# Optimization experiments

Hardware: AMD Instinct MI355X
Metric: run time of the kernel (lower is better)

The kernel has to match this reference:

```python
import jax, jax.numpy as jnp
from jax import lax
import numpy as np

NPOINT = 1024
RADIUS = 0.2
NSAMPLE = 32
MLP = [64, 64, 128]
EPS = 1e-5  # BatchNorm eps (torch default)


def setup_inputs() -> dict:
    key = jax.random.key(0)
    ks = jax.random.split(key, 2 + 3 * len(MLP))
    B, N = 8, 16384
    d = {
        "xyz": jax.random.uniform(ks[0], (B, N, 3), dtype=jnp.float32),
        "points": jax.random.normal(ks[1], (B, N, 3), dtype=jnp.float32),
    }
    cin = 6  # 3 (relative xyz) + 3 (point features)
    for i, cout in enumerate(MLP):
        d[f"w{i}"] = jax.random.normal(ks[2 + i], (cout, cin), dtype=jnp.float32) / np.float32(np.sqrt(cin))
        d[f"b{i}"] = jnp.zeros((cout,), jnp.float32)
        d[f"g{i}"] = jnp.ones((cout,), jnp.float32)
        d[f"be{i}"] = jnp.zeros((cout,), jnp.float32)
        cin = cout
    return d


def _fps(xyz, npoint):
    """Farthest point sampling. xyz: (B,N,3) -> idx (B,npoint) int32.
    Deterministic start at index 0 (original uses a random start)."""
    B, N, _ = xyz.shape

    def step(carry, _):
        distance, farthest = carry  # (B,N), (B,)
        centroid = jnp.take_along_axis(xyz, farthest[:, None, None], axis=1)  # (B,1,3)
        dist = jnp.sum((xyz - centroid) ** 2, axis=-1)  # (B,N)
        distance = jnp.minimum(distance, dist)
        nxt = jnp.argmax(distance, axis=-1).astype(jnp.int32)
        return (distance, nxt), farthest

    init = (jnp.full((B, N), 1e10, xyz.dtype), jnp.zeros((B,), jnp.int32))
    _, idxs = lax.scan(step, init, None, length=npoint)
    return idxs.T  # (B, npoint)


def _gather(points, idx):
    """points: (B,N,C), idx: (B,...) -> (B,...,C)."""
    return jax.vmap(lambda p, i: p[i])(points, idx)


def _ball_query(radius, nsample, xyz, new_xyz):
    B, N, _ = xyz.shape
    # (B,S,N) pairwise squared distances
    sqr = jnp.sum((new_xyz[:, :, None, :] - xyz[:, None, :, :]) ** 2, axis=-1)
    gidx = jnp.where(sqr > radius * radius, N, jnp.arange(N, dtype=jnp.int32))
    gidx = jnp.sort(gidx, axis=-1)[:, :, :nsample]  # (B,S,K)
    # replace out-of-ball (==N) with first in-ball index
    gidx = jnp.where(gidx == N, gidx[:, :, :1], gidx)
    return gidx


def reference(xyz, points, w0, b0, g0, be0, w1, b1, g1, be1, w2, b2, g2, be2):
    B, N, _ = xyz.shape
    fidx = _fps(xyz, NPOINT)                      # (B,S)
    new_xyz = _gather(xyz, fidx)                  # (B,S,3)
    gidx = _ball_query(RADIUS, NSAMPLE, xyz, new_xyz)  # (B,S,K)
    grouped_xyz = _gather(xyz, gidx) - new_xyz[:, :, None, :]  # (B,S,K,3)
    grouped_pts = _gather(points, gidx)           # (B,S,K,C)
    feat = jnp.concatenate([grouped_xyz, grouped_pts], axis=-1)  # (B,S,K,6)
    # shared MLP = 1x1 Conv2d + BatchNorm2d(train-mode stats) + ReLU
    for w, b, g, be in ((w0, b0, g0, be0), (w1, b1, g1, be1), (w2, b2, g2, be2)):
        feat = jnp.einsum('bskc,oc->bsko', feat, w) + b
        mu = feat.mean(axis=(0, 1, 2))
        var = feat.var(axis=(0, 1, 2))  # biased, as torch BN uses for normalization
        feat = jax.nn.relu(g * (feat - mu) * lax.rsqrt(var + EPS) + be)
    new_points = feat.max(axis=2)                 # max over nsample -> (B,S,C_out)
    return new_xyz, new_points
```

## Files before the change

kernel.cpp:

```cpp
#include <hip/hip_runtime.h>
#include <stdint.h>

#pragma clang fp contract(off)

#define NPT   16384
#define BB    8
#define SS    1024
#define KSAMP 32
#define PTOT  (BB*SS*KSAMP)
#define NGRP  (BB*SS)
#define R2    0.04f
#define EPSBN 1e-5f
#define INV_M 3.814697265625e-06f

#define OFF_S1 0
#define OFF_Q1 64
#define OFF_S2 128
#define OFF_Q2 192
#define OFF_S3 256
#define OFF_Q3 384
#define OFF_A1 512
#define OFF_C1 576
#define OFF_A2 640
#define OFF_C2 704
#define OFF_A3 768
#define OFF_C3 896
#define OFF_ZMAX 1024
#define OFF_FEAT (1024 + 1048576)

__device__ __forceinline__ float wave_sum(float v) {
#pragma unroll
  for (int off = 32; off; off >>= 1) v += __shfl_xor(v, off);
  return v;
}
__device__ __forceinline__ float half_max(float v) {
#pragma unroll
  for (int off = 16; off; off >>= 1) v = fmaxf(v, __shfl_xor(v, off));
  return v;
}

__device__ __forceinline__ float wave_max_dpp(float x) {
  int v = __float_as_int(x), t;
  t = __builtin_amdgcn_update_dpp(0, v, 0x111, 0xf, 0xf, true);
  v = __float_as_int(fmaxf(__int_as_float(v), __int_as_float(t)));
  t = __builtin_amdgcn_update_dpp(0, v, 0x112, 0xf, 0xf, true);
  v = __float_as_int(fmaxf(__int_as_float(v), __int_as_float(t)));
  t = __builtin_amdgcn_update_dpp(0, v, 0x114, 0xf, 0xf, true);
  v = __float_as_int(fmaxf(__int_as_float(v), __int_as_float(t)));
  t = __builtin_amdgcn_update_dpp(0, v, 0x118, 0xf, 0xf, true);
  v = __float_as_int(fmaxf(__int_as_float(v), __int_as_float(t)));
  t = __builtin_amdgcn_update_dpp(0, v, 0x142, 0xf, 0xf, true);
  v = __float_as_int(fmaxf(__int_as_float(v), __int_as_float(t)));
  t = __builtin_amdgcn_update_dpp(0, v, 0x143, 0xf, 0xf, true);
  v = __float_as_int(fmaxf(__int_as_float(v), __int_as_float(t)));
  return __int_as_float(__builtin_amdgcn_readlane(v, 63));
}

__global__ __launch_bounds__(1024)
void fps_kernel(const float* __restrict__ xyz, float* __restrict__ newxyz) {
  extern __shared__ float smem[];
  float2* sxy = (float2*)smem;
  __shared__ unsigned bmax[2];
  __shared__ unsigned long long wkey[2];
  const int b = blockIdx.x;
  const int t = threadIdx.x;
  const int lane = t & 63;
  const float* xb = xyz + (size_t)b * NPT * 3;

  float z[16], d[16];
#pragma unroll
  for (int j = 0; j < 16; ++j) {
    int p = j * 1024 + t;
    float xx = xb[3 * p];
    float yy = xb[3 * p + 1];
    float zz = xb[3 * p + 2];
    sxy[p] = make_float2(xx, yy);
    z[j] = zz;
    d[j] = 1e10f;
    asm volatile("" : "+v"(z[j]));
  }

  float cx = xb[0], cy = xb[1], cz = xb[2];
  if (t == 0) {
    bmax[0] = bmax[1] = 0u;
    wkey[0] = wkey[1] = ~0ull;
    float* o = newxyz + (size_t)b * SS * 3;
    o[0] = cx; o[1] = cy; o[2] = cz;
  }
  __syncthreads();

  const float2* pA = sxy + t;
  const float2* pB = sxy + t + 8192;

  for (int it = 1; it < SS; ++it) {
    const int buf = it & 1;
    float bv = 0.0f;
#pragma unroll
    for (int j = 0; j < 16; ++j) {
      float2 xy = (j < 8) ? pA[j * 1024] : pB[(j - 8) * 1024];
      float dx = xy.x - cx, dy = xy.y - cy, dz = z[j] - cz;
      float d2 = (dx * dx + dy * dy) + dz * dz;
      float dm = fminf(d[j], d2);
      d[j] = dm;
      bv = fmaxf(bv, dm);
    }
    float wm = wave_max_dpp(bv);
    if (lane == 0) atomicMax(&bmax[buf], __float_as_uint(wm));
    __syncthreads();
    if (t == 0) { bmax[buf ^ 1] = 0u; wkey[buf ^ 1] = ~0ull; }
    const unsigned bmu = bmax[buf];
    if (__float_as_uint(bv) == bmu) {
      int bj = 0; float zc = z[0];
#pragma unroll
      for (int j = 15; j >= 0; --j)
        if (__float_as_uint(d[j]) == bmu) { bj = j; zc = z[j]; }
      unsigned long long key =
          ((unsigned long long)(unsigned)(bj * 1024 + t) << 32) |
          (unsigned long long)__float_as_uint(zc);
      atomicMin(&wkey[buf], key);
    }
    __syncthreads();
    unsigned long long k = wkey[buf];
    int fi = (int)(unsigned)(k >> 32);
    cz = __uint_as_float((unsigned)k);
    fi = __builtin_amdgcn_readfirstlane(fi);
    float2 cxy = sxy[fi];
    cx = cxy.x; cy = cxy.y;
    if (t == 0) {
      float* o = newxyz + ((size_t)b * SS + it) * 3;
      o[0] = cx; o[1] = cy; o[2] = cz;
    }
  }
}

__global__ __launch_bounds__(256, 2)
void ballq_kernel(const float* __restrict__ xyz, const float* __restrict__ pts,
                  const float* __restrict__ newxyz, float* __restrict__ feat) {
  const int lane = threadIdx.x & 63;
  const int c = blockIdx.x * 4 + (threadIdx.x >> 6);
  const int b = c >> 10;
  const float* xb = xyz + (size_t)b * NPT * 3;
  const float* pb = pts + (size_t)b * NPT * 3;
  const float cx = newxyz[3 * c], cy = newxyz[3 * c + 1], cz = newxyz[3 * c + 2];
  const int base = c * KSAMP;
  const uint64_t ltm = (1ull << lane) - 1ull;

  int cnt = 0, firstp = 0;
  bool haveFirst = false;
  for (int p0 = 0; p0 < NPT && cnt < KSAMP; p0 += 64) {
    int p = p0 + lane;
    float px = xb[3 * p], py = xb[3 * p + 1], pz = xb[3 * p + 2];
    float dx = cx - px, dy = cy - py, dz = cz - pz;
    float sqr = (dx * dx + dy * dy) + dz * dz;
    bool in = (sqr <= R2);
    uint64_t m = __ballot(in);
    if (!haveFirst && m) { firstp = p0 + (__ffsll((unsigned long long)m) - 1); haveFirst = true; }
    int rank = (int)__popcll(m & ltm);
    int slot = cnt + rank;
    if (in && slot < KSAMP) {
      int idx = base + slot;
      feat[0 * PTOT + idx] = px - cx;
      feat[1 * PTOT + idx] = py - cy;
      feat[2 * PTOT + idx] = pz - cz;
      feat[3 * PTOT + idx] = pb[3 * p];
      feat[4 * PTOT + idx] = pb[3 * p + 1];
      feat[5 * PTOT + idx] = pb[3 * p + 2];
    }
    cnt += (int)__popcll(m);
  }
  if (cnt < KSAMP) {
    int slot = cnt + lane;
    if (slot < KSAMP) {
      int idx = base + slot;
      float px = xb[3 * firstp], py = xb[3 * firstp + 1], pz = xb[3 * firstp + 2];
      feat[0 * PTOT + idx] = px - cx;
      feat[1 * PTOT + idx] = py - cy;
      feat[2 * PTOT + idx] = pz - cz;
      feat[3 * PTOT + idx] = pb[3 * firstp];
      feat[4 * PTOT + idx] = pb[3 * firstp + 1];
      feat[5 * PTOT + idx] = pb[3 * firstp + 2];
    }
  }
}

__global__ __launch_bounds__(256, 2)
void mlp1s_kernel(const float* __restrict__ feat, const float* __restrict__ w0,
                  const float* __restrict__ b0, float* __restrict__ stats) {
  float s[64], q[64];
#pragma unroll
  for (int o = 0; o < 64; ++o) { s[o] = 0.0f; q[o] = 0.0f; }
  int gid = blockIdx.x * 256 + threadIdx.x;
  for (int p = gid; p < PTOT; p += 256 * 256) {
    float f[6];
#pragma unroll
    for (int ch = 0; ch < 6; ++ch) f[ch] = feat[ch * PTOT + p];
#pragma unroll
    for (int o = 0; o < 64; ++o) {
      float z = b0[o];
#pragma unroll
      for (int i = 0; i < 6; ++i) z = fmaf(w0[o * 6 + i], f[i], z);
      s[o] += z; q[o] = fmaf(z, z, q[o]);
    }
  }
  const int lane = threadIdx.x & 63;
#pragma unroll
  for (int o = 0; o < 64; ++o) { s[o] = wave_sum(s[o]); q[o] = wave_sum(q[o]); }
  __shared__ float ls[128];
  if (threadIdx.x < 128) ls[threadIdx.x] = 0.0f;
  __syncthreads();
  if (lane == 0) {
#pragma unroll
    for (int o = 0; o < 64; ++o) { atomicAdd(&ls[o], s[o]); atomicAdd(&ls[64 + o], q[o]); }
  }
  __syncthreads();
  if (threadIdx.x < 64) atomicAdd(&stats[OFF_S1 + threadIdx.x], ls[threadIdx.x]);
  else if (threadIdx.x < 128) atomicAdd(&stats[OFF_Q1 + threadIdx.x - 64], ls[threadIdx.x]);
}

__global__ void fin_kernel(const float* __restrict__ g, const float* __restrict__ be,
                           const float* __restrict__ s, const float* __restrict__ q,
                           float* __restrict__ A, float* __restrict__ C, int Cn) {
  int o = blockIdx.x * blockDim.x + threadIdx.x;
  if (o >= Cn) return;
  float mu = s[o] * INV_M;
  float var = q[o] * INV_M - mu * mu;
  float a = g[o] / sqrtf(var + EPSBN);
  A[o] = a;
  C[o] = be[o] - a * mu;
}

__global__ __launch_bounds__(256, 2)
void mlp2s_kernel(const float* __restrict__ feat,
                  const float* __restrict__ w0, const float* __restrict__ b0,
                  const float* __restrict__ w1, const float* __restrict__ b1,
                  const float* __restrict__ par, float* __restrict__ stats) {
  const float* a1 = par + OFF_A1;
  const float* c1 = par + OFF_C1;
  const int lane = threadIdx.x & 63;
  float sp = 0.0f, qp = 0.0f;
  int gid = blockIdx.x * 256 + threadIdx.x;
  for (int p = gid; p < PTOT; p += 512 * 256) {
    float f[6];
#pragma unroll
    for (int ch = 0; ch < 6; ++ch) f[ch] = feat[ch * PTOT + p];
    float h1[64];
#pragma unroll
    for (int o = 0; o < 64; ++o) {
      float z = b0[o];
#pragma unroll
      for (int i = 0; i < 6; ++i) z = fmaf(w0[o * 6 + i], f[i], z);
      h1[o] = fmaxf(fmaf(a1[o], z, c1[o]), 0.0f);
    }
    for (int o = 0; o < 64; o += 2) {
      float z0 = b1[o], z1 = b1[o + 1];
#pragma unroll
      for (int i = 0; i < 64; ++i) {
        z0 = fmaf(w1[o * 64 + i], h1[i], z0);
        z1 = fmaf(w1[(o + 1) * 64 + i], h1[i], z1);
      }
      float s0 = wave_sum(z0), q0 = wave_sum(z0 * z0);
      float s1 = wave_sum(z1), q1 = wave_sum(z1 * z1);
      if (lane == o)     { sp += s0; qp += q0; }
      if (lane == o + 1) { sp += s1; qp += q1; }
    }
  }
  atomicAdd(&stats[OFF_S2 + lane], sp);
  atomicAdd(&stats[OFF_Q2 + lane], qp);
}

__global__ __launch_bounds__(256, 2)
void mlp3f_kernel(const float* __restrict__ feat,
                  const float* __restrict__ w0, const float* __restrict__ b0,
                  const float* __restrict__ w1, const float* __restrict__ b1,
                  const float* __restrict__ w2, const float* __restrict__ b2,
                  const float* __restrict__ par, float* __restrict__ stats,
                  float* __restrict__ zmax) {
  const float* a1 = par + OFF_A1;
  const float* c1 = par + OFF_C1;
  const float* a2 = par + OFF_A2;
  const float* c2 = par + OFF_C2;
  const int lane = threadIdx.x & 63;
  float sp0 = 0.0f, qp0 = 0.0f;
  float sp1 = 0.0f, qp1 = 0.0f;
  int gid = blockIdx.x * 256 + threadIdx.x;
  for (int p = gid; p < PTOT; p += 512 * 256) {
    float f[6];
#pragma unroll
    for (int ch = 0; ch < 6; ++ch) f[ch] = feat[ch * PTOT + p];
    float h2[64];
#pragma unroll
    for (int o = 0; o < 64; ++o) h2[o] = b1[o];
    for (int i = 0; i < 64; ++i) {
      float z = b0[i];
#pragma unroll
      for (int ch = 0; ch < 6; ++ch) z = fmaf(w0[i * 6 + ch], f[ch], z);
      float h1i = fmaxf(fmaf(a1[i], z, c1[i]), 0.0f);
#pragma unroll
      for (int o = 0; o < 64; ++o) h2[o] = fmaf(w1[o * 64 + i], h1i, h2[o]);
    }
#pragma unroll
    for (int o = 0; o < 64; ++o) h2[o] = fmaxf(fmaf(a2[o], h2[o], c2[o]), 0.0f);

    const int g = p >> 5;
    for (int o = 0; o < 128; o += 2) {
      float z0 = b2[o], z1 = b2[o + 1];
#pragma unroll
      for (int i = 0; i < 64; ++i) {
        z0 = fmaf(w2[o * 64 + i], h2[i], z0);
        z1 = fmaf(w2[(o + 1) * 64 + i], h2[i], z1);
      }
      float s0 = wave_sum(z0), q0 = wave_sum(z0 * z0);
      float s1 = wave_sum(z1), q1 = wave_sum(z1 * z1);
      if (lane == (o & 63))       { if (o < 64) { sp0 += s0; qp0 += q0; } else { sp1 += s0; qp1 += q0; } }
      if (lane == ((o + 1) & 63)) { if (o < 64) { sp0 += s1; qp0 += q1; } else { sp1 += s1; qp1 += q1; } }
      float m0 = half_max(z0), m1 = half_max(z1);
      if ((lane & 31) == (o & 31))       zmax[g * 128 + o]     = m0;
      if ((lane & 31) == ((o + 1) & 31)) zmax[g * 128 + o + 1] = m1;
    }
  }
  atomicAdd(&stats[OFF_S3 + lane], sp0);
  atomicAdd(&stats[OFF_Q3 + lane], qp0);
  atomicAdd(&stats[OFF_S3 + 64 + lane], sp1);
  atomicAdd(&stats[OFF_Q3 + 64 + lane], qp1);
}

__global__ __launch_bounds__(256, 4)
void final_out_kernel(const float* __restrict__ zmax, const float* __restrict__ par,
                      float* __restrict__ out2) {
  const float* a3 = par + OFF_A3;
  const float* c3 = par + OFF_C3;
  int idx = blockIdx.x * 256 + threadIdx.x;
  int c = idx & 127;
  out2[idx] = fmaxf(fmaf(a3[c], zmax[idx], c3[c]), 0.0f);
}

extern "C" void kernel_launch(void* const* d_in, const int* in_sizes, int n_in,
                              void* d_out, int out_size, void* d_ws, size_t ws_size,
                              hipStream_t stream) {
  const float* xyz = (const float*)d_in[0];
  const float* pts = (const float*)d_in[1];
  const float* w0  = (const float*)d_in[2];
  const float* b0  = (const float*)d_in[3];
  const float* g0  = (const float*)d_in[4];
  const float* be0 = (const float*)d_in[5];
  const float* w1  = (const float*)d_in[6];
  const float* b1  = (const float*)d_in[7];
  const float* g1  = (const float*)d_in[8];
  const float* be1 = (const float*)d_in[9];
  const float* w2  = (const float*)d_in[10];
  const float* b2  = (const float*)d_in[11];
  const float* g2  = (const float*)d_in[12];
  const float* be2 = (const float*)d_in[13];

  float* out  = (float*)d_out;
  float* nxz  = out;
  float* out2 = out + BB * SS * 3;

  float* ws    = (float*)d_ws;
  float* stats = ws;
  float* par   = ws;
  float* zmax  = ws + OFF_ZMAX;
  float* feat  = ws + OFF_FEAT;

  hipMemsetAsync(stats, 0, 512 * sizeof(float), stream);

  fps_kernel<<<BB, 1024, NPT * sizeof(float2), stream>>>(xyz, nxz);
  ballq_kernel<<<2048, 256, 0, stream>>>(xyz, pts, nxz, feat);

  mlp1s_kernel<<<256, 256, 0, stream>>>(feat, w0, b0, stats);
  fin_kernel<<<1, 64, 0, stream>>>(g0, be0, stats + OFF_S1, stats + OFF_Q1,
                                   par + OFF_A1, par + OFF_C1, 64);
  mlp2s_kernel<<<512, 256, 0, stream>>>(feat, w0, b0, w1, b1, par, stats);
  fin_kernel<<<1, 64, 0, stream>>>(g1, be1, stats + OFF_S2, stats + OFF_Q2,
                                   par + OFF_A2, par + OFF_C2, 64);
  mlp3f_kernel<<<512, 256, 0, stream>>>(feat, w0, b0, w1, b1, w2, b2, par, stats, zmax);
  fin_kernel<<<1, 128, 0, stream>>>(g2, be2, stats + OFF_S3, stats + OFF_Q3,
                                    par + OFF_A3, par + OFF_C3, 128);
  final_out_kernel<<<4096, 256, 0, stream>>>(zmax, par, out2);
}
```

Baseline: 2.114 ms.

## Keep all FPS coordinates in registers with packed math and a single-atomic argmax

The farthest-point-sampling kernel now holds x, y, z and distance for each thread's 16 points in packed two-wide float registers, so the shared-memory xy array is gone. Distance updates use packed float2 arithmetic. The argmax across the block now packs the max distance and the inverted index into one 64-bit key, found with a wave-level DPP min plus one atomicMax per wave. The winning thread publishes its coordinates through shared memory, which removes one atomic round and the shared-memory lookup of the centroid. In exchange, register pressure rises, and there are still two barriers per iteration.

New measurement: 2.726 ms. 28.9% more time.

```diff
diff --git a/kernel.cpp b/kernel.cpp
--- a/kernel.cpp
+++ b/kernel.cpp
@@ -28,6 +28,8 @@
 #define OFF_ZMAX 1024
 #define OFF_FEAT (1024 + 1048576)
 
+typedef float f32x2 __attribute__((ext_vector_type(2)));
+
 __device__ __forceinline__ float wave_sum(float v) {
 #pragma unroll
   for (int off = 32; off; off >>= 1) v += __shfl_xor(v, off);
@@ -56,76 +58,104 @@
   return __int_as_float(__builtin_amdgcn_readlane(v, 63));
 }
 
-__global__ __launch_bounds__(1024)
+__device__ __forceinline__ unsigned wave_min_u32_dpp(unsigned x) {
+  unsigned v = x, t;
+  t = (unsigned)__builtin_amdgcn_update_dpp(-1, (int)v, 0x111, 0xf, 0xf, false);
+  v = v < t ? v : t;
+  t = (unsigned)__builtin_amdgcn_update_dpp(-1, (int)v, 0x112, 0xf, 0xf, false);
+  v = v < t ? v : t;
+  t = (unsigned)__builtin_amdgcn_update_dpp(-1, (int)v, 0x114, 0xf, 0xf, false);
+  v = v < t ? v : t;
+  t = (unsigned)__builtin_amdgcn_update_dpp(-1, (int)v, 0x118, 0xf, 0xf, false);
+  v = v < t ? v : t;
+  t = (unsigned)__builtin_amdgcn_update_dpp(-1, (int)v, 0x142, 0xf, 0xf, false);
+  v = v < t ? v : t;
+  t = (unsigned)__builtin_amdgcn_update_dpp(-1, (int)v, 0x143, 0xf, 0xf, false);
+  v = v < t ? v : t;
+  return (unsigned)__builtin_amdgcn_readlane((int)v, 63);
+}
+
+__global__ __launch_bounds__(1024, 4)
 void fps_kernel(const float* __restrict__ xyz, float* __restrict__ newxyz) {
-  extern __shared__ float smem[];
-  float2* sxy = (float2*)smem;
-  __shared__ unsigned bmax[2];
   __shared__ unsigned long long wkey[2];
+  __shared__ float cpub[2][3];
   const int b = blockIdx.x;
   const int t = threadIdx.x;
   const int lane = t & 63;
   const float* xb = xyz + (size_t)b * NPT * 3;
 
-  float z[16], d[16];
-#pragma unroll
-  for (int j = 0; j < 16; ++j) {
-    int p = j * 1024 + t;
-    float xx = xb[3 * p];
-    float yy = xb[3 * p + 1];
-    float zz = xb[3 * p + 2];
-    sxy[p] = make_float2(xx, yy);
-    z[j] = zz;
-    d[j] = 1e10f;
-    asm volatile("" : "+v"(z[j]));
+  f32x2 X[8], Y[8], Z[8], D[8];
+#pragma unroll
+  for (int i = 0; i < 8; ++i) {
+    int p0 = (2 * i) * 1024 + t;
+    int p1 = (2 * i + 1) * 1024 + t;
+    X[i] = (f32x2){xb[3 * p0], xb[3 * p1]};
+    Y[i] = (f32x2){xb[3 * p0 + 1], xb[3 * p1 + 1]};
+    Z[i] = (f32x2){xb[3 * p0 + 2], xb[3 * p1 + 2]};
+    D[i] = (f32x2){1e10f, 1e10f};
+    asm volatile("" : "+v"(X[i]), "+v"(Y[i]), "+v"(Z[i]));
   }
 
   float cx = xb[0], cy = xb[1], cz = xb[2];
   if (t == 0) {
-    bmax[0] = bmax[1] = 0u;
-    wkey[0] = wkey[1] = ~0ull;
+    wkey[0] = 0ull; wkey[1] = 0ull;
     float* o = newxyz + (size_t)b * SS * 3;
     o[0] = cx; o[1] = cy; o[2] = cz;
   }
   __syncthreads();
 
-  const float2* pA = sxy + t;
-  const float2* pB = sxy + t + 8192;
-
   for (int it = 1; it < SS; ++it) {
     const int buf = it & 1;
-    float bv = 0.0f;
-#pragma unroll
-    for (int j = 0; j < 16; ++j) {
-      float2 xy = (j < 8) ? pA[j * 1024] : pB[(j - 8) * 1024];
-      float dx = xy.x - cx, dy = xy.y - cy, dz = z[j] - cz;
-      float d2 = (dx * dx + dy * dy) + dz * dz;
-      float dm = fminf(d[j], d2);
-      d[j] = dm;
-      bv = fmaxf(bv, dm);
-    }
-    float wm = wave_max_dpp(bv);
-    if (lane == 0) atomicMax(&bmax[buf], __float_as_uint(wm));
+    const float ncx = -cx, ncy = -cy, ncz = -cz;
+    const f32x2 vx = (f32x2){ncx, ncx};
+    const f32x2 vy = (f32x2){ncy, ncy};
+    const f32x2 vz = (f32x2){ncz, ncz};
+    float bv0 = 0.0f, bv1 = 0.0f;
+#pragma unroll
+    for (int i = 0; i < 8; ++i) {
+      f32x2 dx = X[i] + vx;
+      f32x2 dy = Y[i] + vy;
+      f32x2 dz = Z[i] + vz;
+      f32x2 d2 = (dx * dx + dy * dy) + dz * dz;
+      float m0 = fminf(D[i].x, d2.x);
+      float m1 = fminf(D[i].y, d2.y);
+      D[i].x = m0; D[i].y = m1;
+      bv0 = fmaxf(bv0, m0);
+      bv1 = fmaxf(bv1, m1);
+    }
+    const float bv = fmaxf(bv0, bv1);
+    const float wm = wave_max_dpp(bv);
+
+    unsigned cand = 0xffffffffu;
+    float xc = 0.f, yc = 0.f, zc = 0.f;
+    if (bv == wm) {
+      int bj = 0;
+#pragma unroll
+      for (int j = 15; j >= 0; --j) {
+        float dj = (j & 1) ? D[j >> 1].y : D[j >> 1].x;
+        if (dj == wm) {
+          bj = j;
+          xc = (j & 1) ? X[j >> 1].y : X[j >> 1].x;
+          yc = (j & 1) ? Y[j >> 1].y : Y[j >> 1].x;
+          zc = (j & 1) ? Z[j >> 1].y : Z[j >> 1].x;
+        }
+      }
+      cand = (unsigned)(bj * 1024 + t);
+    }
+    const unsigned wmin = wave_min_u32_dpp(cand);
+    if (lane == 0)
+      atomicMax(&wkey[buf],
+                ((unsigned long long)__float_as_uint(wm) << 32) |
+                (unsigned long long)(unsigned)~wmin);
     __syncthreads();
-    if (t == 0) { bmax[buf ^ 1] = 0u; wkey[buf ^ 1] = ~0ull; }
-    const unsigned bmu = bmax[buf];
-    if (__float_as_uint(bv) == bmu) {
-      int bj = 0; float zc = z[0];
-#pragma unroll
-      for (int j = 15; j >= 0; --j)
-        if (__float_as_uint(d[j]) == bmu) { bj = j; zc = z[j]; }
-      unsigned long long key =
-          ((unsigned long long)(unsigned)(bj * 1024 + t) << 32) |
-          (unsigned long long)__float_as_uint(zc);
-      atomicMin(&wkey[buf], key);
+    const unsigned long long k = wkey[buf];
+    const int fi = (int)~(unsigned)k;
+    if (t == 0) wkey[buf ^ 1] = 0ull;
+    if (cand == (unsigned)fi) {
+      cpub[buf][0] = xc; cpub[buf][1] = yc; cpub[buf][2] = zc;
     }
     __syncthreads();
-    unsigned long long k = wkey[buf];
-    int fi = (int)(unsigned)(k >> 32);
-    cz = __uint_as_float((unsigned)k);
-    fi = __builtin_amdgcn_readfirstlane(fi);
-    float2 cxy = sxy[fi];
-    cx = cxy.x; cy = cxy.y;
+    cx = cpub[buf][0]; cy = cpub[buf][1]; cz = cpub[buf][2];
     if (t == 0) {
       float* o = newxyz + ((size_t)b * SS + it) * 3;
       o[0] = cx; o[1] = cy; o[2] = cz;
@@ -364,7 +394,7 @@
 
   hipMemsetAsync(stats, 0, 512 * sizeof(float), stream);
 
-  fps_kernel<<<BB, 1024, NPT * sizeof(float2), stream>>>(xyz, nxz);
+  fps_kernel<<<BB, 1024, 0, stream>>>(xyz, nxz);
   ballq_kernel<<<2048, 256, 0, stream>>>(xyz, pts, nxz, feat);
 
   mlp1s_kernel<<<256, 256, 0, stream>>>(feat, w0, b0, stats);
```
